# Performance work log

Measured on AMD Instinct MI355X. Metric: run time of the kernel, lower is better.

The kernel has to match this reference:

```python
import jax, jax.numpy as jnp
import numpy as np
import math

B, S, D, H = 2, 2048, 1024, 16
HD = D // H  # head_dims = 64


def setup_inputs() -> dict:
    key = jax.random.key(0)
    ks = jax.random.split(key, 8)
    sc = 1.0 / math.sqrt(D)
    return {
        "queries": jax.random.normal(ks[0], (B, S, D), jnp.float32),
        "keys":    jax.random.normal(ks[1], (B, S, D), jnp.float32),
        "values":  jax.random.normal(ks[2], (B, S, D), jnp.float32),
        # causal mask: 1 where attending allowed, 0 where blocked (masked_fill on ==0)
        "mask": jnp.tril(jnp.ones((S, S), jnp.int32)),
        "Wq": jax.random.normal(ks[3], (D, D), jnp.float32) * sc,
        "bq": jnp.zeros((D,), jnp.float32),
        "Wk": jax.random.normal(ks[4], (D, D), jnp.float32) * sc,
        "bk": jnp.zeros((D,), jnp.float32),
        "Wv": jax.random.normal(ks[5], (D, D), jnp.float32) * sc,
        "bv": jnp.zeros((D,), jnp.float32),
        "Wo": jax.random.normal(ks[6], (D, D), jnp.float32) * sc,
        "bo": jnp.zeros((D,), jnp.float32),
    }


def _split_heads(x):
    # (B, S, D) -> (B, H, S, HD)
    return x.reshape(B, S, H, HD).transpose(0, 2, 1, 3)


def reference(queries, keys, values, mask, Wq, bq, Wk, bk, Wv, bv, Wo, bo):
    q = queries @ Wq + bq
    k = keys @ Wk + bk
    # NOTE: faithful to source quirk — V is projected from the ALREADY-PROJECTED keys
    # (original: keys = self.W_keys(keys); values = self.W_values(keys))
    v = k @ Wv + bv
    q, k, v = _split_heads(q), _split_heads(k), _split_heads(v)
    # naive full NxN attention, as in the source
    scores = jnp.einsum("bhqd,bhkd->bhqk", q, k) / math.sqrt(HD)
    scores = jnp.where(mask == 0, jnp.float32(-1e9), scores)
    probs = jax.nn.softmax(scores, axis=-1)
    attn = jnp.einsum("bhqk,bhkd->bhqd", probs, v)
    attn = attn.transpose(0, 2, 1, 3).reshape(B, S, D)
    return attn @ Wo + bo
```

## Files before the change

### kernel.cpp

```cpp
#include <hip/hip_runtime.h>

typedef unsigned short u16;
typedef unsigned int u32;
typedef __bf16 bf16x8 __attribute__((ext_vector_type(8)));
typedef float f32x4 __attribute__((ext_vector_type(4)));

#define MFMA16(a, b, c) __builtin_amdgcn_mfma_f32_16x16x32_bf16(a, b, c, 0, 0, 0)

__device__ __forceinline__ void gload16(const void* g, void* l) {
  __builtin_amdgcn_global_load_lds((const __attribute__((address_space(1))) void*)g,
                                   (__attribute__((address_space(3))) void*)l, 16, 0, 0);
}

__device__ __forceinline__ u16 f2bf(float f) {
  u32 u = __builtin_bit_cast(u32, f);
  u += 0x7fffu + ((u >> 16) & 1u);
  return (u16)(u >> 16);
}
__device__ __forceinline__ u32 pack2(float a, float b) {
  return (u32)f2bf(a) | ((u32)f2bf(b) << 16);
}

__global__ __launch_bounds__(256) void cvt_kernel(const float* __restrict__ q,
                                                  const float* __restrict__ k,
                                                  u16* __restrict__ qb,
                                                  u16* __restrict__ kb) {
  const float* src = blockIdx.y ? k : q;
  u16* dst = blockIdx.y ? kb : qb;
  size_t i = (size_t)blockIdx.x * 256 + threadIdx.x;
  float4 v = ((const float4*)src)[i];
  ushort4 o;
  o.x = f2bf(v.x); o.y = f2bf(v.y); o.z = f2bf(v.z); o.w = f2bf(v.w);
  ((ushort4*)dst)[i] = o;
}

__global__ __launch_bounds__(256) void wtrans_kernel(const float* W0, const float* W1,
                                                     const float* W2, const float* W3,
                                                     u16* T0, u16* T1, u16* T2, u16* T3) {
  int z = blockIdx.z;
  const float* W = z == 0 ? W0 : z == 1 ? W1 : z == 2 ? W2 : W3;
  u16* T = z == 0 ? T0 : z == 1 ? T1 : z == 2 ? T2 : T3;
  __shared__ float tile[64][65];
  int tr = blockIdx.y * 64, tc = blockIdx.x * 64;
  int tid = threadIdx.x;
  int c4 = (tid & 15) * 4, r0 = tid >> 4;
#pragma unroll
  for (int i = 0; i < 4; i++) {
    int r = r0 + i * 16;
    float4 v = *(const float4*)(W + (size_t)(tr + r) * 1024 + tc + c4);
    tile[r][c4 + 0] = v.x; tile[r][c4 + 1] = v.y;
    tile[r][c4 + 2] = v.z; tile[r][c4 + 3] = v.w;
  }
  __syncthreads();
#pragma unroll
  for (int i = 0; i < 2; i++) {
    int c = tid + i * 256;
    int n = c >> 3, kg = c & 7;
    uint4 o;
    o.x = pack2(tile[kg * 8 + 0][n], tile[kg * 8 + 1][n]);
    o.y = pack2(tile[kg * 8 + 2][n], tile[kg * 8 + 3][n]);
    o.z = pack2(tile[kg * 8 + 4][n], tile[kg * 8 + 5][n]);
    o.w = pack2(tile[kg * 8 + 6][n], tile[kg * 8 + 7][n]);
    *(uint4*)(T + (size_t)(tc + n) * 1024 + tr + kg * 8) = o;
  }
}

template <int MODE>
__global__ __launch_bounds__(256) void gemm_kernel(
    const u16* __restrict__ A, const u16* __restrict__ Bt,
    const float* __restrict__ bias, void* __restrict__ Cout,
    float scale, int M, int N, int K) {
  __shared__ __attribute__((aligned(16))) char sAB[12288];
  char* sA = sAB;
  char* sB = sAB + 8192;
  const int tid = threadIdx.x, lane = tid & 63, w = tid >> 6;
  const int l15 = lane & 15, quad = lane >> 4;
  const int wm = (w >> 1) * 64, wn = (w & 1) * 32;
  const int m0 = blockIdx.y * 128, n0 = blockIdx.x * 64;

  const int srA0 = w * 32 + (lane >> 2), srA1 = srA0 + 16, srB = w * 16 + (lane >> 2);
  const u16* aP0 = A + (size_t)(m0 + srA0) * K + ((lane & 3) ^ ((srA0 >> 1) & 3)) * 8;
  const u16* aP1 = A + (size_t)(m0 + srA1) * K + ((lane & 3) ^ ((srA1 >> 1) & 3)) * 8;
  const u16* bP  = Bt + (size_t)(n0 + srB) * K + ((lane & 3) ^ ((srB >> 1) & 3)) * 8;
  char* lA0 = sA + w * 2048; char* lA1 = lA0 + 1024;
  char* lB  = sB + w * 1024;

  int aoff[4], boff[2];
#pragma unroll
  for (int t = 0; t < 4; t++) {
    int ra = wm + t * 16 + l15;
    aoff[t] = ra * 64 + ((quad ^ ((ra >> 1) & 3)) * 16);
  }
#pragma unroll
  for (int t = 0; t < 2; t++) {
    int rb = wn + t * 16 + l15;
    boff[t] = rb * 64 + ((quad ^ ((rb >> 1) & 3)) * 16);
  }

  f32x4 acc[4][2] = {};
  for (int k = 0; k < K; k += 32) {
    __syncthreads();
    gload16(aP0, lA0); gload16(aP1, lA1); gload16(bP, lB);
    aP0 += 32; aP1 += 32; bP += 32;
    __syncthreads();
    bf16x8 af[4], bfr[2];
#pragma unroll
    for (int t = 0; t < 4; t++) af[t] = *(const bf16x8*)(sA + aoff[t]);
#pragma unroll
    for (int t = 0; t < 2; t++) bfr[t] = *(const bf16x8*)(sB + boff[t]);
#pragma unroll
    for (int mt = 0; mt < 4; mt++)
#pragma unroll
      for (int nt = 0; nt < 2; nt++)
        acc[mt][nt] = MFMA16(af[mt], bfr[nt], acc[mt][nt]);
  }

#pragma unroll
  for (int nt = 0; nt < 2; nt++) {
    int col = n0 + wn + nt * 16 + l15;
    float bv = bias[col];
#pragma unroll
    for (int mt = 0; mt < 4; mt++) {
      int row = m0 + wm + mt * 16 + quad * 4;
      if (MODE == 0) {
        u16* C = (u16*)Cout;
#pragma unroll
        for (int r = 0; r < 4; r++)
          C[(size_t)(row + r) * N + col] = f2bf((acc[mt][nt][r] + bv) * scale);
      } else if (MODE == 1) {
        u16* C = (u16*)Cout;
        int hh = col >> 6, hd = col & 63;
        int bb = row >> 11, s = row & 2047;
        ushort4 o;
        o.x = f2bf((acc[mt][nt][0] + bv) * scale);
        o.y = f2bf((acc[mt][nt][1] + bv) * scale);
        o.z = f2bf((acc[mt][nt][2] + bv) * scale);
        o.w = f2bf((acc[mt][nt][3] + bv) * scale);
        *(ushort4*)(C + ((size_t)((bb * 16 + hh) * 64 + hd) * 2048 + s)) = o;
      } else {
        float* C = (float*)Cout;
#pragma unroll
        for (int r = 0; r < 4; r++)
          C[(size_t)(row + r) * N + col] = (acc[mt][nt][r] + bv) * scale;
      }
    }
  }
}

__global__ __launch_bounds__(256) void attn_kernel(const u16* __restrict__ qw,
                                                   const u16* __restrict__ kw,
                                                   const u16* __restrict__ vw,
                                                   u16* __restrict__ aout) {
  __shared__ __attribute__((aligned(16))) char sQ[8192];
  __shared__ __attribute__((aligned(16))) char sKV[2][16384];
  __shared__ __attribute__((aligned(16))) char sP[8192];
  const int p = blockIdx.x, bh = blockIdx.y;
  const int b = bh >> 4, h = bh & 15;
  const int tid = threadIdx.x, lane = tid & 63, w = tid >> 6;
  const int l15 = lane & 15, quad = lane >> 4;
  const u16* kb0 = kw + (size_t)(b * 2048) * 1024 + h * 64;
  const u16* vb0 = vw + (size_t)bh * 64 * 2048;

  for (int phase = 0; phase < 2; ++phase) {
    const int t = phase ? (31 - p) : p;
    __syncthreads();
    {
      const u16* qbase = qw + (size_t)(b * 2048 + t * 64) * 1024 + h * 64;
#pragma unroll
      for (int i = 0; i < 2; i++) {
        int c = tid + i * 256, row = c >> 3, cg = c & 7;
        *(uint4*)(sQ + row * 128 + ((cg ^ (row & 7)) * 16)) =
            *(const uint4*)(qbase + (size_t)row * 1024 + cg * 8);
      }
    }
    {
#pragma unroll
      for (int i = 0; i < 2; i++) {
        int c = tid + i * 256, row = c >> 3, cg = c & 7;
        int d = row * 128 + ((cg ^ (row & 7)) * 16);
        *(uint4*)(sKV[0] + d) = *(const uint4*)(kb0 + (size_t)row * 1024 + cg * 8);
        *(uint4*)(sKV[0] + 8192 + d) = *(const uint4*)(vb0 + (size_t)row * 2048 + cg * 8);
      }
    }

    float lsum = 0.f;
    f32x4 o[4] = {};
    for (int j = 0; j <= t; ++j) {
      __syncthreads();
      if (j < t) {
        char* dstb = sKV[(j + 1) & 1];
#pragma unroll
        for (int i = 0; i < 2; i++) {
          int c = tid + i * 256, row = c >> 3, cg = c & 7;
          int d = row * 128 + ((cg ^ (row & 7)) * 16);
          *(uint4*)(dstb + d) =
              *(const uint4*)(kb0 + (size_t)((j + 1) * 64 + row) * 1024 + cg * 8);
          *(uint4*)(dstb + 8192 + d) =
              *(const uint4*)(vb0 + (size_t)row * 2048 + (j + 1) * 64 + cg * 8);
        }
      }
      const char* sK = sKV[j & 1];
      const char* sV = sK + 8192;

      f32x4 st[4] = {};
#pragma unroll
      for (int kt = 0; kt < 2; ++kt) {
        bf16x8 kf[4], qf;
        {
          int row = w * 16 + l15;
          qf = *(const bf16x8*)(sQ + row * 128 + (((kt * 4 + quad) ^ (row & 7)) * 16));
        }
#pragma unroll
        for (int mt = 0; mt < 4; mt++) {
          int row = mt * 16 + l15;
          kf[mt] = *(const bf16x8*)(sK + row * 128 + (((kt * 4 + quad) ^ (row & 7)) * 16));
        }
#pragma unroll
        for (int mt = 0; mt < 4; mt++) st[mt] = MFMA16(kf[mt], qf, st[mt]);
      }

      const bool dmask = (j == t);
      const int qcol = w * 16 + l15;
      float e[4][4];
#pragma unroll
      for (int mt = 0; mt < 4; mt++)
#pragma unroll
        for (int r = 0; r < 4; r++) {
          float ev = __builtin_amdgcn_exp2f(st[mt][r]);
          if (dmask && (mt * 16 + quad * 4 + r > qcol)) ev = 0.f;
          e[mt][r] = ev;
          lsum += ev;
        }

      {
        int qrow = l15;
#pragma unroll
        for (int mt = 0; mt < 4; mt++) {
          u32 lo = pack2(e[mt][0], e[mt][1]);
          u32 hi = pack2(e[mt][2], e[mt][3]);
          int cgp = (2 * mt + (quad >> 1)) ^ (qrow & 7);
          *(uint2*)(sP + w * 2048 + qrow * 128 + cgp * 16 + (quad & 1) * 8) =
              make_uint2(lo, hi);
        }
      }
      __syncthreads();

#pragma unroll
      for (int kt = 0; kt < 2; ++kt) {
        bf16x8 vf[4], pf;
        {
          int qrow = l15;
          pf = *(const bf16x8*)(sP + w * 2048 + qrow * 128 +
                                (((kt * 4 + quad) ^ (qrow & 7)) * 16));
        }
#pragma unroll
        for (int mt = 0; mt < 4; mt++) {
          int row = mt * 16 + l15;
          vf[mt] = *(const bf16x8*)(sV + row * 128 + (((kt * 4 + quad) ^ (row & 7)) * 16));
        }
#pragma unroll
        for (int mt = 0; mt < 4; mt++) o[mt] = MFMA16(vf[mt], pf, o[mt]);
      }
    }

    lsum += __shfl_xor(lsum, 16, 64);
    lsum += __shfl_xor(lsum, 32, 64);
    float inv = 1.0f / lsum;
    int token = b * 2048 + t * 64 + w * 16 + l15;
#pragma unroll
    for (int mt = 0; mt < 4; mt++) {
      int d0 = h * 64 + mt * 16 + quad * 4;
      ushort4 ov;
      ov.x = f2bf(o[mt][0] * inv);
      ov.y = f2bf(o[mt][1] * inv);
      ov.z = f2bf(o[mt][2] * inv);
      ov.w = f2bf(o[mt][3] * inv);
      *(ushort4*)(aout + (size_t)token * 1024 + d0) = ov;
    }
  }
}

extern "C" void kernel_launch(void* const* d_in, const int* in_sizes, int n_in,
                              void* d_out, int out_size, void* d_ws, size_t ws_size,
                              hipStream_t stream) {
  const float* queries = (const float*)d_in[0];
  const float* keys    = (const float*)d_in[1];
  const float* Wq = (const float*)d_in[4];
  const float* bq = (const float*)d_in[5];
  const float* Wk = (const float*)d_in[6];
  const float* bk = (const float*)d_in[7];
  const float* Wv = (const float*)d_in[8];
  const float* bv = (const float*)d_in[9];
  const float* Wo = (const float*)d_in[10];
  const float* bo = (const float*)d_in[11];

  char* ws = (char*)d_ws;
  u16* qb  = (u16*)(ws);
  u16* kb  = (u16*)(ws + (8u << 20));
  u16* qP  = (u16*)(ws + (16u << 20));
  u16* kP  = (u16*)(ws);
  u16* vP  = (u16*)(ws + (8u << 20));
  u16* WqT = (u16*)(ws + (24u << 20));
  u16* WkT = (u16*)(ws + (26u << 20));
  u16* WvT = (u16*)(ws + (28u << 20));
  u16* WoT = (u16*)(ws + (30u << 20));

  const float kscale = 1.4426950408889634f / 8.0f;

  cvt_kernel<<<dim3(4096, 2), 256, 0, stream>>>(queries, keys, qb, kb);
  wtrans_kernel<<<dim3(16, 16, 4), 256, 0, stream>>>(Wq, Wk, Wv, Wo, WqT, WkT, WvT, WoT);
  gemm_kernel<0><<<dim3(16, 32), 256, 0, stream>>>(qb, WqT, bq, qP, kscale, 4096, 1024, 1024);
  gemm_kernel<0><<<dim3(16, 32), 256, 0, stream>>>(kb, WkT, bk, kP, 1.0f, 4096, 1024, 1024);
  gemm_kernel<1><<<dim3(16, 32), 256, 0, stream>>>(kP, WvT, bv, vP, 1.0f, 4096, 1024, 1024);
  attn_kernel<<<dim3(16, 32), 256, 0, stream>>>(qP, kP, vP, qP);
  gemm_kernel<2><<<dim3(16, 32), 256, 0, stream>>>(qP, WoT, bo, d_out, 1.0f, 4096, 1024, 1024);
}
```

Baseline: 264.3 us.

## Batch Q/K projections, widen GEMM K-step, use async LDS loads in attention

The Q and K projection GEMMs are merged into one launch by selecting operand sets on blockIdx.z. The GEMM K-step doubles from 32 to 64, with a 128-byte-row XOR swizzle, which halves barrier pairs per tile and doubles shared memory use. The attention kernel swaps register-staged uint4 copies for direct global-to-LDS loads, issues the next K/V prefetch after the P barrier, and swaps the grid axes so consecutive blocks walk heads. Risks include lower occupancy from the larger LDS footprint and a race if the prefetched buffer is still being read.

Result: faster. 233.7 us (-11.6%).

```diff
diff --git a/kernel.cpp b/kernel.cpp
--- a/kernel.cpp
+++ b/kernel.cpp
@@ -67,52 +67,70 @@
 
 template <int MODE>
 __global__ __launch_bounds__(256) void gemm_kernel(
-    const u16* __restrict__ A, const u16* __restrict__ Bt,
-    const float* __restrict__ bias, void* __restrict__ Cout,
-    float scale, int M, int N, int K) {
-  __shared__ __attribute__((aligned(16))) char sAB[12288];
+    const u16* A0, const u16* B0, const float* bias0, void* C0, float scale0,
+    const u16* A1, const u16* B1, const float* bias1, void* C1, float scale1,
+    int M, int N, int K) {
+  const u16* A = A0; const u16* Bt = B0; const float* bias = bias0; void* Cout = C0;
+  float scale = scale0;
+  if (blockIdx.z) { A = A1; Bt = B1; bias = bias1; Cout = C1; scale = scale1; }
+
+  __shared__ __attribute__((aligned(16))) char sAB[24576];
   char* sA = sAB;
-  char* sB = sAB + 8192;
+  char* sB = sAB + 16384;
   const int tid = threadIdx.x, lane = tid & 63, w = tid >> 6;
   const int l15 = lane & 15, quad = lane >> 4;
   const int wm = (w >> 1) * 64, wn = (w & 1) * 32;
   const int m0 = blockIdx.y * 128, n0 = blockIdx.x * 64;
 
-  const int srA0 = w * 32 + (lane >> 2), srA1 = srA0 + 16, srB = w * 16 + (lane >> 2);
-  const u16* aP0 = A + (size_t)(m0 + srA0) * K + ((lane & 3) ^ ((srA0 >> 1) & 3)) * 8;
-  const u16* aP1 = A + (size_t)(m0 + srA1) * K + ((lane & 3) ^ ((srA1 >> 1) & 3)) * 8;
-  const u16* bP  = Bt + (size_t)(n0 + srB) * K + ((lane & 3) ^ ((srB >> 1) & 3)) * 8;
-  char* lA0 = sA + w * 2048; char* lA1 = lA0 + 1024;
-  char* lB  = sB + w * 1024;
+  const int lrow = lane >> 3, lcg = (lane & 7) ^ lrow;
+  const u16* aP[4]; const u16* bP[2];
+  char *lA[4], *lB[2];
+#pragma unroll
+  for (int i = 0; i < 4; i++) {
+    int r = w * 32 + i * 8 + lrow;
+    aP[i] = A + (size_t)(m0 + r) * K + lcg * 8;
+    lA[i] = sA + w * 4096 + i * 1024;
+  }
+#pragma unroll
+  for (int i = 0; i < 2; i++) {
+    int r = w * 16 + i * 8 + lrow;
+    bP[i] = Bt + (size_t)(n0 + r) * K + lcg * 8;
+    lB[i] = sB + w * 2048 + i * 1024;
+  }
 
   int aoff[4], boff[2];
 #pragma unroll
   for (int t = 0; t < 4; t++) {
     int ra = wm + t * 16 + l15;
-    aoff[t] = ra * 64 + ((quad ^ ((ra >> 1) & 3)) * 16);
+    aoff[t] = ra * 128 + ((quad ^ (ra & 7)) * 16);
   }
 #pragma unroll
   for (int t = 0; t < 2; t++) {
     int rb = wn + t * 16 + l15;
-    boff[t] = rb * 64 + ((quad ^ ((rb >> 1) & 3)) * 16);
+    boff[t] = rb * 128 + ((quad ^ (rb & 7)) * 16);
   }
 
   f32x4 acc[4][2] = {};
-  for (int k = 0; k < K; k += 32) {
+  for (int k = 0; k < K; k += 64) {
     __syncthreads();
-    gload16(aP0, lA0); gload16(aP1, lA1); gload16(bP, lB);
-    aP0 += 32; aP1 += 32; bP += 32;
+#pragma unroll
+    for (int i = 0; i < 4; i++) { gload16(aP[i], lA[i]); aP[i] += 64; }
+#pragma unroll
+    for (int i = 0; i < 2; i++) { gload16(bP[i], lB[i]); bP[i] += 64; }
     __syncthreads();
-    bf16x8 af[4], bfr[2];
-#pragma unroll
-    for (int t = 0; t < 4; t++) af[t] = *(const bf16x8*)(sA + aoff[t]);
-#pragma unroll
-    for (int t = 0; t < 2; t++) bfr[t] = *(const bf16x8*)(sB + boff[t]);
-#pragma unroll
-    for (int mt = 0; mt < 4; mt++)
-#pragma unroll
-      for (int nt = 0; nt < 2; nt++)
-        acc[mt][nt] = MFMA16(af[mt], bfr[nt], acc[mt][nt]);
+#pragma unroll
+    for (int kt = 0; kt < 2; kt++) {
+      bf16x8 af[4], bfr[2];
+#pragma unroll
+      for (int t = 0; t < 4; t++) af[t] = *(const bf16x8*)(sA + (aoff[t] ^ (kt * 64)));
+#pragma unroll
+      for (int t = 0; t < 2; t++) bfr[t] = *(const bf16x8*)(sB + (boff[t] ^ (kt * 64)));
+#pragma unroll
+      for (int mt = 0; mt < 4; mt++)
+#pragma unroll
+        for (int nt = 0; nt < 2; nt++)
+          acc[mt][nt] = MFMA16(af[mt], bfr[nt], acc[mt][nt]);
+    }
   }
 
 #pragma unroll
@@ -154,10 +172,11 @@
   __shared__ __attribute__((aligned(16))) char sQ[8192];
   __shared__ __attribute__((aligned(16))) char sKV[2][16384];
   __shared__ __attribute__((aligned(16))) char sP[8192];
-  const int p = blockIdx.x, bh = blockIdx.y;
+  const int bh = blockIdx.x, p = blockIdx.y;
   const int b = bh >> 4, h = bh & 15;
   const int tid = threadIdx.x, lane = tid & 63, w = tid >> 6;
   const int l15 = lane & 15, quad = lane >> 4;
+  const int lrow = lane >> 3, lcg = (lane & 7) ^ lrow;
   const u16* kb0 = kw + (size_t)(b * 2048) * 1024 + h * 64;
   const u16* vb0 = vw + (size_t)bh * 64 * 2048;
 
@@ -168,18 +187,10 @@
       const u16* qbase = qw + (size_t)(b * 2048 + t * 64) * 1024 + h * 64;
 #pragma unroll
       for (int i = 0; i < 2; i++) {
-        int c = tid + i * 256, row = c >> 3, cg = c & 7;
-        *(uint4*)(sQ + row * 128 + ((cg ^ (row & 7)) * 16)) =
-            *(const uint4*)(qbase + (size_t)row * 1024 + cg * 8);
-      }
-    }
-    {
-#pragma unroll
-      for (int i = 0; i < 2; i++) {
-        int c = tid + i * 256, row = c >> 3, cg = c & 7;
-        int d = row * 128 + ((cg ^ (row & 7)) * 16);
-        *(uint4*)(sKV[0] + d) = *(const uint4*)(kb0 + (size_t)row * 1024 + cg * 8);
-        *(uint4*)(sKV[0] + 8192 + d) = *(const uint4*)(vb0 + (size_t)row * 2048 + cg * 8);
+        int r = w * 16 + i * 8 + lrow;
+        gload16(qbase + (size_t)r * 1024 + lcg * 8, sQ + w * 2048 + i * 1024);
+        gload16(kb0 + (size_t)r * 1024 + lcg * 8, sKV[0] + w * 2048 + i * 1024);
+        gload16(vb0 + (size_t)r * 2048 + lcg * 8, sKV[0] + 8192 + w * 2048 + i * 1024);
       }
     }
 
@@ -187,18 +198,6 @@
     f32x4 o[4] = {};
     for (int j = 0; j <= t; ++j) {
       __syncthreads();
-      if (j < t) {
-        char* dstb = sKV[(j + 1) & 1];
-#pragma unroll
-        for (int i = 0; i < 2; i++) {
-          int c = tid + i * 256, row = c >> 3, cg = c & 7;
-          int d = row * 128 + ((cg ^ (row & 7)) * 16);
-          *(uint4*)(dstb + d) =
-              *(const uint4*)(kb0 + (size_t)((j + 1) * 64 + row) * 1024 + cg * 8);
-          *(uint4*)(dstb + 8192 + d) =
-              *(const uint4*)(vb0 + (size_t)row * 2048 + (j + 1) * 64 + cg * 8);
-        }
-      }
       const char* sK = sKV[j & 1];
       const char* sV = sK + 8192;
 
@@ -244,6 +243,18 @@
         }
       }
       __syncthreads();
+
+      if (j < t) {
+        char* dstb = sKV[(j + 1) & 1];
+#pragma unroll
+        for (int i = 0; i < 2; i++) {
+          int r = w * 16 + i * 8 + lrow;
+          gload16(kb0 + (size_t)((j + 1) * 64 + r) * 1024 + lcg * 8,
+                  dstb + w * 2048 + i * 1024);
+          gload16(vb0 + (size_t)r * 2048 + (j + 1) * 64 + lcg * 8,
+                  dstb + 8192 + w * 2048 + i * 1024);
+        }
+      }
 
 #pragma unroll
       for (int kt = 0; kt < 2; ++kt) {
@@ -309,9 +320,11 @@
 
   cvt_kernel<<<dim3(4096, 2), 256, 0, stream>>>(queries, keys, qb, kb);
   wtrans_kernel<<<dim3(16, 16, 4), 256, 0, stream>>>(Wq, Wk, Wv, Wo, WqT, WkT, WvT, WoT);
-  gemm_kernel<0><<<dim3(16, 32), 256, 0, stream>>>(qb, WqT, bq, qP, kscale, 4096, 1024, 1024);
-  gemm_kernel<0><<<dim3(16, 32), 256, 0, stream>>>(kb, WkT, bk, kP, 1.0f, 4096, 1024, 1024);
-  gemm_kernel<1><<<dim3(16, 32), 256, 0, stream>>>(kP, WvT, bv, vP, 1.0f, 4096, 1024, 1024);
-  attn_kernel<<<dim3(16, 32), 256, 0, stream>>>(qP, kP, vP, qP);
-  gemm_kernel<2><<<dim3(16, 32), 256, 0, stream>>>(qP, WoT, bo, d_out, 1.0f, 4096, 1024, 1024);
-}
+  gemm_kernel<0><<<dim3(16, 32, 2), 256, 0, stream>>>(
+      qb, WqT, bq, qP, kscale, kb, WkT, bk, kP, 1.0f, 4096, 1024, 1024);
+  gemm_kernel<1><<<dim3(16, 32, 1), 256, 0, stream>>>(
+      kP, WvT, bv, vP, 1.0f, kP, WvT, bv, vP, 1.0f, 4096, 1024, 1024);
+  attn_kernel<<<dim3(32, 16), 256, 0, stream>>>(qP, kP, vP, qP);
+  gemm_kernel<2><<<dim3(16, 32, 1), 256, 0, stream>>>(
+      qP, WoT, bo, d_out, 1.0f, qP, WoT, bo, d_out, 1.0f, 4096, 1024, 1024);
+}
```
